# Kernel tuning notes

Measured on AMD Instinct MI355X. Metric: run time of the kernel, lower is better.

The kernel has to match this reference:

```python
import jax, jax.numpy as jnp
import numpy as np

B, N, D, S = 128, 1024, 512, 64
ITERS = 3
EPS = 1e-8


def setup_inputs() -> dict:
    key = jax.random.key(0)
    ks = jax.random.split(key, 10)
    inp = {
        "inputs_pe": jax.random.normal(ks[0], (B, N, D), dtype=jnp.float32),
        "inputs": jax.random.normal(ks[1], (B, N, D), dtype=jnp.float32),
        "slots": jax.random.normal(ks[2], (1, S, D), dtype=jnp.float32),
        "W1": jax.random.normal(ks[3], (D, D), dtype=jnp.float32) * 0.02,
        "b1": jnp.zeros((D,), dtype=jnp.float32),
        "W2": jax.random.normal(ks[4], (D, D), dtype=jnp.float32) * 0.02,
        "b2": jnp.zeros((D,), dtype=jnp.float32),
        "W3": jax.random.normal(ks[5], (D, D), dtype=jnp.float32) * 0.02,
        "b3": jnp.zeros((D,), dtype=jnp.float32),
    }
    return inp


def reference(inputs_pe, inputs, slots, W1, b1, W2, b2, W3, b3):
    b = inputs_pe.shape[0]
    scale = D ** (-0.5)
    # to_k: Linear -> ReLU -> Linear -> ReLU -> Linear (torch Linear: x @ W.T + b)
    h = jax.nn.relu(jnp.einsum('bnd,ed->bne', inputs_pe, W1) + b1)
    h = jax.nn.relu(jnp.einsum('bnd,ed->bne', h, W2) + b2)
    k = jnp.einsum('bnd,ed->bne', h, W3) + b3  # [b, n, d]

    q = jnp.broadcast_to(slots, (b, S, D))  # slots never updated in the loop
    for _ in range(ITERS):
        dots = jnp.einsum('bid,bjd->bij', q, k) * scale  # [b, S, n]
        s_j = dots.sum(axis=2, keepdims=True)            # sum over keys j -> [b, S, 1]
        s_all = dots.sum(axis=(1, 2), keepdims=True)     # total per batch -> [b, 1, 1]
        dots = dots / s_j * s_all
        attn = jax.nn.sigmoid(dots)
        attn2 = attn / (attn.sum(axis=-1, keepdims=True) + EPS)
        updates = jnp.einsum('bjd,bij->bid', inputs, attn2)  # [b, S, d]
    return updates, attn
```

## Files before the change

### kernel.cpp

```cpp
#include <hip/hip_runtime.h>
#include <stdint.h>

#define Bb 128
#define Nn 1024
#define Dd 512
#define Ss 64

constexpr float kScale = 0.044194173824159216f;
constexpr float kEps = 1e-8f;

typedef __bf16 bf16x8 __attribute__((ext_vector_type(8)));
typedef float f32x4 __attribute__((ext_vector_type(4)));
typedef float f32x16 __attribute__((ext_vector_type(16)));
typedef unsigned short ushort8 __attribute__((ext_vector_type(8)));

#define MFMA32 __builtin_amdgcn_mfma_f32_32x32x16_bf16

__device__ inline unsigned short f2bf_rne(float x) {
  unsigned u = __builtin_bit_cast(unsigned, x);
  u += 0x7FFFu + ((u >> 16) & 1u);
  return (unsigned short)(u >> 16);
}
__device__ inline float bf2f(unsigned short h) {
  unsigned u = ((unsigned)h) << 16;
  return __builtin_bit_cast(float, u);
}

__device__ inline void gl_lds16(const void* g, void* l) {
  typedef unsigned int u32;
  auto gp = (u32 __attribute__((address_space(1)))*)(unsigned long long)(uintptr_t)g;
  auto lp = (u32 __attribute__((address_space(3)))*)(unsigned int)(uintptr_t)l;
  __builtin_amdgcn_global_load_lds(gp, lp, 16, 0, 0);
}

__global__ void cast_split_i(const float* __restrict__ in,
                             unsigned short* __restrict__ out, int n8) {
  int i = blockIdx.x * blockDim.x + threadIdx.x;
  const int stride = gridDim.x * blockDim.x;
  for (; i < n8; i += stride) {
    const float4 v0 = ((const float4*)in)[i * 2];
    const float4 v1 = ((const float4*)in)[i * 2 + 1];
    float f[8] = {v0.x, v0.y, v0.z, v0.w, v1.x, v1.y, v1.z, v1.w};
    ushort8 h, lo;
#pragma unroll
    for (int j = 0; j < 8; j++) {
      h[j] = f2bf_rne(f[j]);
      lo[j] = f2bf_rne(f[j] - bf2f(h[j]));
    }
    ((ushort8*)out)[i * 2] = h;
    ((ushort8*)out)[i * 2 + 1] = lo;
  }
}

template <int ACT>
__global__ __launch_bounds__(512, 1) void gemm_hp(
    const unsigned short* __restrict__ A, const unsigned short* __restrict__ W,
    const float* __restrict__ bias, unsigned short* __restrict__ C) {
  constexpr int NH = 32;
  extern __shared__ unsigned short lds[];
  const int t = threadIdx.x, l = t & 63, w = t >> 6;
  const int wr = w >> 2, wc = w & 3;

  const int wg = ((blockIdx.x & 7) << 7) + (blockIdx.x >> 3);
  const long rowA0 = (long)(wg >> 1) * 256;
  const int colB0 = (wg & 1) * 256;

  const unsigned short* base8 = (w < 4) ? A + rowA0 * 1024 : W + (long)colB0 * 1024;
  const int p2s = ((l >> 1) ^ (l >> 4)) & 1;
  const unsigned short* srcp[4];
  int dstp[4];
#pragma unroll
  for (int j = 0; j < 4; j++) {
    const int cid = (w & 3) * 4 + j;
    srcp[j] = base8 + (long)(cid * 16 + (l >> 2)) * 1024 + p2s * 16 + (l & 1) * 8;
    dstp[j] = (w * 4 + j) * 512;
  }
#define STG(h)                                                            \
  {                                                                       \
    unsigned short* bq_ = lds + ((h) & 3) * 16384;                        \
    _Pragma("unroll") for (int j = 0; j < 4; j++)                         \
        gl_lds16(srcp[j] + (h) * 32, bq_ + dstp[j]);                      \
  }

  const int pp16 = (((l >> 5) ^ ((l >> 2) & 1))) * 16;
  const int abase0 = (wr * 128 + (l & 31)) * 32 + pp16;
  const int bbase0 = 8192 + (wc * 64 + (l & 31)) * 32 + pp16;

#define READF(h, S)                                                       \
  {                                                                       \
    const unsigned short* bq_ = lds + ((h) & 3) * 16384;                  \
    _Pragma("unroll") for (int m = 0; m < 4; m++) {                       \
      ah##S[m] = *(const bf16x8*)(bq_ + abase0 + m * 1024);               \
      al##S[m] = *(const bf16x8*)(bq_ + abase0 + m * 1024 + 8);           \
    }                                                                     \
    _Pragma("unroll") for (int n = 0; n < 2; n++) {                       \
      bh##S[n] = *(const bf16x8*)(bq_ + bbase0 + n * 1024);               \
      bl##S[n] = *(const bf16x8*)(bq_ + bbase0 + n * 1024 + 8);           \
    }                                                                     \
  }

#define MFMACL(S)                                                         \
  {                                                                       \
    _Pragma("unroll") for (int m = 0; m < 4; m++)                         \
        _Pragma("unroll") for (int n = 0; n < 2; n++) {                   \
      acc[m][n] = MFMA32(ah##S[m], bh##S[n], acc[m][n], 0, 0, 0);         \
      acc[m][n] = MFMA32(al##S[m], bh##S[n], acc[m][n], 0, 0, 0);         \
      acc[m][n] = MFMA32(ah##S[m], bl##S[n], acc[m][n], 0, 0, 0);         \
    }                                                                     \
  }

#define BODY(h, CUR, NXT)                                                 \
  {                                                                       \
    asm volatile("s_waitcnt lgkmcnt(0)" ::: "memory");                    \
    __builtin_amdgcn_sched_barrier(0);                                    \
    if ((h) < 29) {                                                       \
      asm volatile("s_waitcnt vmcnt(8)" ::: "memory");                    \
    } else if ((h) == 29) {                                               \
      asm volatile("s_waitcnt vmcnt(4)" ::: "memory");                    \
    } else if ((h) == 30) {                                               \
      asm volatile("s_waitcnt vmcnt(0)" ::: "memory");                    \
    }                                                                     \
    __builtin_amdgcn_s_barrier();                                         \
    if ((h) + 4 < NH) STG((h) + 4);                                       \
    if ((h) + 1 < NH) READF((h) + 1, NXT);                                \
    __builtin_amdgcn_sched_barrier(0);                                    \
    __builtin_amdgcn_s_setprio(1);                                        \
    MFMACL(CUR);                                                          \
    __builtin_amdgcn_s_setprio(0);                                        \
  }

  f32x16 acc[4][2] = {};
  bf16x8 ahA[4], alA[4], bhA[2], blA[2];
  bf16x8 ahB[4], alB[4], bhB[2], blB[2];

  STG(0); STG(1); STG(2); STG(3);
  asm volatile("s_waitcnt vmcnt(12)" ::: "memory");
  __builtin_amdgcn_s_barrier();
  READF(0, A);

  for (int hh = 0; hh < NH; hh += 2) {
    BODY(hh, A, B);
    BODY(hh + 1, B, A);
  }
#undef STG
#undef READF
#undef MFMACL
#undef BODY

#pragma unroll
  for (int m = 0; m < 4; m++)
#pragma unroll
    for (int n = 0; n < 2; n++) {
      const int col = colB0 + wc * 64 + n * 32 + (l & 31);
      const float bv = bias[col];
      const int cofs = (col >> 3) * 16 + (col & 7);
#pragma unroll
      for (int r = 0; r < 16; r++) {
        const long row = rowA0 + wr * 128 + m * 32 + (r & 3) + 8 * (r >> 2) + 4 * (l >> 5);
        float xv = acc[m][n][r] + bv;
        if (ACT) xv = fmaxf(xv, 0.0f);
        const unsigned short h = f2bf_rne(xv);
        unsigned short* cp = C + row * 1024 + cofs;
        cp[0] = h;
        cp[8] = f2bf_rne(xv - bf2f(h));
      }
    }
}

__global__ __launch_bounds__(256) void gemm_dots_split(
    const unsigned short* __restrict__ QI, const unsigned short* __restrict__ KI,
    float* __restrict__ dots) {
  constexpr int K = 512, BM = 64, BN = 128, BK = 32;
  __shared__ __align__(16) unsigned short lah[BM * BK];
  __shared__ __align__(16) unsigned short lal[BM * BK];
  __shared__ __align__(16) unsigned short lbh[BN * BK];
  __shared__ __align__(16) unsigned short lbl[BN * BK];
  const int t = threadIdx.x, l = t & 63, w = t >> 6;
  const int b = blockIdx.x >> 3, bc = blockIdx.x & 7;
  const unsigned short* kb = KI + (long)b * Nn * 1024;
  f32x4 acc[4][2] = {};

  const int qbase = (t >> 2) * 1024 + (t & 3) * 16;
  const long kbase0 = (long)(bc * BN + (t >> 2)) * 1024 + (t & 3) * 16;
  const long kbase1 = (long)(bc * BN + 64 + (t >> 2)) * 1024 + (t & 3) * 16;

  for (int k0 = 0; k0 < K; k0 += BK) {
    const int ko = k0 * 2;
    const int lo = w * 512;
    gl_lds16(QI + qbase + ko, lah + lo);
    gl_lds16(QI + qbase + ko + 8, lal + lo);
    gl_lds16(kb + kbase0 + ko, lbh + lo);
    gl_lds16(kb + kbase0 + ko + 8, lbl + lo);
    gl_lds16(kb + kbase1 + ko, lbh + 2048 + lo);
    gl_lds16(kb + kbase1 + ko + 8, lbl + 2048 + lo);
    __syncthreads();
    bf16x8 ah[4], al[4], bh[2], bl[2];
#pragma unroll
    for (int m = 0; m < 4; m++) {
      const int off = (m * 16 + (l & 15)) * BK + (l >> 4) * 8;
      ah[m] = *(const bf16x8*)(lah + off);
      al[m] = *(const bf16x8*)(lal + off);
    }
#pragma unroll
    for (int n = 0; n < 2; n++) {
      const int off = (w * 32 + n * 16 + (l & 15)) * BK + (l >> 4) * 8;
      bh[n] = *(const bf16x8*)(lbh + off);
      bl[n] = *(const bf16x8*)(lbl + off);
    }
#pragma unroll
    for (int m = 0; m < 4; m++)
#pragma unroll
      for (int n = 0; n < 2; n++) {
        acc[m][n] = __builtin_amdgcn_mfma_f32_16x16x32_bf16(ah[m], bh[n], acc[m][n], 0, 0, 0);
        acc[m][n] = __builtin_amdgcn_mfma_f32_16x16x32_bf16(al[m], bh[n], acc[m][n], 0, 0, 0);
        acc[m][n] = __builtin_amdgcn_mfma_f32_16x16x32_bf16(ah[m], bl[n], acc[m][n], 0, 0, 0);
      }
    __syncthreads();
  }
  float* dp = dots + (long)b * Ss * Nn;
#pragma unroll
  for (int m = 0; m < 4; m++) {
    const int row = m * 16 + (l >> 4) * 4;
#pragma unroll
    for (int n = 0; n < 2; n++) {
      const int col = bc * BN + w * 32 + n * 16 + (l & 15);
#pragma unroll
      for (int r = 0; r < 4; r++) dp[(long)(row + r) * Nn + col] = acc[m][n][r] * kScale;
    }
  }
}

__global__ __launch_bounds__(256) void reduce_k(
    const float* __restrict__ dots, float* __restrict__ s_j, float* __restrict__ s_all) {
  const int b = blockIdx.x;
  const int t = threadIdx.x;
  const float* dp = dots + (long)b * Ss * Nn;
  const int i = t >> 2, qq = t & 3;
  float s = 0.f;
  const float* rp = dp + i * Nn + qq * 256;
  for (int j = 0; j < 256; j++) s += rp[j];
  __shared__ float part[256];
  __shared__ float rowsum[64];
  part[t] = s;
  __syncthreads();
  if (t < 64) {
    const float v = part[t * 4] + part[t * 4 + 1] + part[t * 4 + 2] + part[t * 4 + 3];
    rowsum[t] = v;
    s_j[b * 64 + t] = v;
  }
  __syncthreads();
  if (t == 0) {
    float tot = 0.f;
    for (int k = 0; k < 64; k++) tot += rowsum[k];
    s_all[b] = tot;
  }
}

__global__ __launch_bounds__(256) void attn_k(
    const float* __restrict__ dots, const float* __restrict__ s_j,
    const float* __restrict__ s_all, float* __restrict__ attn_out,
    float* __restrict__ inv_r) {
  const int bi = blockIdx.x;
  const int b = bi >> 6;
  const int t = threadIdx.x;
  const float ratio = s_all[b] / s_j[bi];
  const float* dp = dots + (long)bi * Nn;
  float* ap = attn_out + (long)bi * Nn;
  float s = 0.f;
#pragma unroll
  for (int qq = 0; qq < 4; qq++) {
    const int j = qq * 256 + t;
    const float x = dp[j] * ratio;
    const float a = 1.f / (1.f + expf(-x));
    ap[j] = a;
    s += a;
  }
  __shared__ float red[256];
  red[t] = s;
  __syncthreads();
  for (int off = 128; off > 0; off >>= 1) {
    if (t < off) red[t] += red[t + off];
    __syncthreads();
  }
  if (t == 0) inv_r[bi] = 1.f / (red[0] + kEps);
}

__global__ __launch_bounds__(256, 1) void updates_k2(
    const float* __restrict__ attn, const float* __restrict__ inputs,
    const float* __restrict__ inv_r, float* __restrict__ out0) {
  constexpr int NT2 = 32;
  constexpr int BUF_F = 10240;
  extern __shared__ float ldsf[];
  const int t = threadIdx.x, lam = t & 63, w = t >> 6;
  const int b = blockIdx.x >> 1, dt = blockIdx.x & 1;
  const int ig = t >> 5, dg = t & 31;
  const float* inb = inputs + (size_t)b * (Nn * Dd) + dt * 256;
  const float* attsrc = attn + (size_t)b * (Ss * Nn) + (size_t)(t >> 2) * Nn + (t & 3) * 8;
  float acc[8][8] = {};
  float4 ga0, ga1, gb0, gb1;

#define UISSUE(bufi, tile, G0, G1)                                        \
  {                                                                       \
    const int j0_ = (tile)*32;                                            \
    G0 = *(const float4*)(attsrc + j0_);                                  \
    G1 = *(const float4*)(attsrc + j0_ + 4);                              \
    float* db_ = ldsf + (bufi)*BUF_F;                                     \
    _Pragma("unroll") for (int i_ = 0; i_ < 8; i_++) {                    \
      const int row_ = i_ * 4 + w;                                        \
      gl_lds16(inb + (size_t)(j0_ + row_) * Dd + lam * 4, db_ + row_ * 256); \
    }                                                                     \
  }

#define UWRITE(bufi, G0, G1)                                              \
  {                                                                       \
    float* ab_ = ldsf + (bufi)*BUF_F + 8192;                              \
    const int col_ = t >> 2;                                              \
    const int r0_ = (t & 3) * 8;                                          \
    ab_[(r0_ + 0) * 64 + col_] = G0.x;                                    \
    ab_[(r0_ + 1) * 64 + col_] = G0.y;                                    \
    ab_[(r0_ + 2) * 64 + col_] = G0.z;                                    \
    ab_[(r0_ + 3) * 64 + col_] = G0.w;                                    \
    ab_[(r0_ + 4) * 64 + col_] = G1.x;                                    \
    ab_[(r0_ + 5) * 64 + col_] = G1.y;                                    \
    ab_[(r0_ + 6) * 64 + col_] = G1.z;                                    \
    ab_[(r0_ + 7) * 64 + col_] = G1.w;                                    \
  }

#define UCOMP(bufi)                                                       \
  {                                                                       \
    const float* db_ = ldsf + (bufi)*BUF_F;                               \
    const float* ab_ = db_ + 8192;                                        \
    _Pragma("unroll 4") for (int jj = 0; jj < 32; jj++) {                 \
      float av[8], vv[8];                                                 \
      *(float4*)&av[0] = *(const float4*)(ab_ + jj * 64 + ig * 8);        \
      *(float4*)&av[4] = *(const float4*)(ab_ + jj * 64 + ig * 8 + 4);    \
      *(float4*)&vv[0] = *(const float4*)(db_ + jj * 256 + dg * 8);       \
      *(float4*)&vv[4] = *(const float4*)(db_ + jj * 256 + dg * 8 + 4);   \
      _Pragma("unroll") for (int m_ = 0; m_ < 8; m_++)                    \
          _Pragma("unroll") for (int n_ = 0; n_ < 8; n_++)                \
              acc[m_][n_] = __builtin_fmaf(av[m_], vv[n_], acc[m_][n_]);  \
    }                                                                     \
  }

  UISSUE(0, 0, ga0, ga1);
  UISSUE(1, 1, gb0, gb1);
  UWRITE(0, ga0, ga1);

  for (int tt = 0; tt < NT2; tt += 2) {
    asm volatile("s_waitcnt vmcnt(10)" ::: "memory");
    UWRITE((tt + 1) % 3, gb0, gb1);
    asm volatile("s_waitcnt lgkmcnt(0)" ::: "memory");
    __builtin_amdgcn_s_barrier();
    __builtin_amdgcn_sched_barrier(0);
    if (tt < NT2 - 2) UISSUE((tt + 2) % 3, tt + 2, ga0, ga1);
    UCOMP(tt % 3);
    if (tt + 1 < NT2 - 1) {
      asm volatile("s_waitcnt vmcnt(10)" ::: "memory");
    } else {
      asm volatile("s_waitcnt vmcnt(0)" ::: "memory");
    }
    if (tt + 1 < NT2 - 1) UWRITE((tt + 2) % 3, ga0, ga1);
    asm volatile("s_waitcnt lgkmcnt(0)" ::: "memory");
    __builtin_amdgcn_s_barrier();
    __builtin_amdgcn_sched_barrier(0);
    if (tt + 1 < NT2 - 2) UISSUE((tt + 3) % 3, tt + 3, gb0, gb1);
    UCOMP((tt + 1) % 3);
  }
#undef UISSUE
#undef UWRITE
#undef UCOMP

#pragma unroll
  for (int m = 0; m < 8; m++) {
    const int i = ig * 8 + m;
    const float ir = inv_r[b * 64 + i];
    float4 o0, o1;
    o0.x = acc[m][0] * ir; o0.y = acc[m][1] * ir; o0.z = acc[m][2] * ir; o0.w = acc[m][3] * ir;
    o1.x = acc[m][4] * ir; o1.y = acc[m][5] * ir; o1.z = acc[m][6] * ir; o1.w = acc[m][7] * ir;
    float* op = out0 + (size_t)(b * 64 + i) * Dd + dt * 256 + dg * 8;
    *(float4*)op = o0;
    *(float4*)(op + 4) = o1;
  }
}

extern "C" void kernel_launch(void* const* d_in, const int* in_sizes, int n_in,
                              void* d_out, int out_size, void* d_ws, size_t ws_size,
                              hipStream_t stream) {
  (void)in_sizes; (void)n_in; (void)out_size; (void)ws_size;
  const float* inputs_pe = (const float*)d_in[0];
  const float* inputs = (const float*)d_in[1];
  const float* slots = (const float*)d_in[2];
  const float* W1 = (const float*)d_in[3];
  const float* b1 = (const float*)d_in[4];
  const float* W2 = (const float*)d_in[5];
  const float* b2 = (const float*)d_in[6];
  const float* W3 = (const float*)d_in[7];
  const float* b3 = (const float*)d_in[8];

  char* ws = (char*)d_ws;
  size_t off = 0;
  auto alloc = [&](size_t bytes) -> void* {
    void* p = ws + off;
    off += (bytes + 255) & ~(size_t)255;
    return p;
  };
  const size_t actB = (size_t)Bb * Nn * 1024 * 2;
  unsigned short* AI = (unsigned short*)alloc(actB);
  unsigned short* BI = (unsigned short*)alloc(actB);
  unsigned short* w1i = (unsigned short*)alloc(Dd * 1024 * 2);
  unsigned short* w2i = (unsigned short*)alloc(Dd * 1024 * 2);
  unsigned short* w3i = (unsigned short*)alloc(Dd * 1024 * 2);
  unsigned short* qi = (unsigned short*)alloc(Ss * 1024 * 2);
  float* dotsb = (float*)alloc((size_t)Bb * Ss * Nn * 4);
  float* s_j = (float*)alloc(Bb * Ss * 4);
  float* s_all = (float*)alloc(Bb * 4);
  float* inv_r = (float*)alloc(Bb * Ss * 4);

  float* out_updates = (float*)d_out;
  float* out_attn = out_updates + (size_t)Bb * Ss * Dd;

  const int kLdsG = 4 * 32 * 1024;
  const int kLdsU = 3 * 40 * 1024;
  hipFuncSetAttribute(reinterpret_cast<const void*>(gemm_hp<1>),
                      hipFuncAttributeMaxDynamicSharedMemorySize, kLdsG);
  hipFuncSetAttribute(reinterpret_cast<const void*>(gemm_hp<0>),
                      hipFuncAttributeMaxDynamicSharedMemorySize, kLdsG);
  hipFuncSetAttribute(reinterpret_cast<const void*>(updates_k2),
                      hipFuncAttributeMaxDynamicSharedMemorySize, kLdsU);

  cast_split_i<<<4096, 256, 0, stream>>>(inputs_pe, AI, Bb * Nn * Dd / 8);
  cast_split_i<<<128, 256, 0, stream>>>(W1, w1i, Dd * Dd / 8);
  cast_split_i<<<128, 256, 0, stream>>>(W2, w2i, Dd * Dd / 8);
  cast_split_i<<<128, 256, 0, stream>>>(W3, w3i, Dd * Dd / 8);
  cast_split_i<<<16, 256, 0, stream>>>(slots, qi, Ss * Dd / 8);

  gemm_hp<1><<<1024, 512, kLdsG, stream>>>(AI, w1i, b1, BI);
  gemm_hp<1><<<1024, 512, kLdsG, stream>>>(BI, w2i, b2, AI);
  gemm_hp<0><<<1024, 512, kLdsG, stream>>>(AI, w3i, b3, BI);

  gemm_dots_split<<<Bb * 8, 256, 0, stream>>>(qi, BI, dotsb);
  reduce_k<<<Bb, 256, 0, stream>>>(dotsb, s_j, s_all);
  attn_k<<<Bb * Ss, 256, 0, stream>>>(dotsb, s_j, s_all, out_attn, inv_r);
  updates_k2<<<Bb * 2, 256, kLdsU, stream>>>(out_attn, inputs, inv_r, out_updates);
}
```

Baseline: 1.030 ms.

## Shrink GEMM and updates tiles, restructure reduce with wave shuffles

The three MLP GEMMs move from 256x256 tiles on 512-thread blocks to 128x128 tiles on 256-thread blocks with two blocks per CU, and the LDS swizzle is changed to match. The updates kernel now splits D into four 128-wide slices over 16-row tiles, so it launches more blocks with a smaller LDS footprint. The reduce kernel switches to coalesced float4 row reads with wavefront shuffle reductions. The aim is more parallelism and occupancy and less uncoalesced reading, at the cost of less data reuse per tile in the GEMMs and more redundant attention loads in the updates kernel.

```diff
diff --git a/kernel.cpp b/kernel.cpp
--- a/kernel.cpp
+++ b/kernel.cpp
@@ -53,55 +53,57 @@
 }
 
 template <int ACT>
-__global__ __launch_bounds__(512, 1) void gemm_hp(
+__global__ __launch_bounds__(256, 2) void gemm_tp(
     const unsigned short* __restrict__ A, const unsigned short* __restrict__ W,
     const float* __restrict__ bias, unsigned short* __restrict__ C) {
   constexpr int NH = 32;
   extern __shared__ unsigned short lds[];
   const int t = threadIdx.x, l = t & 63, w = t >> 6;
-  const int wr = w >> 2, wc = w & 3;
-
-  const int wg = ((blockIdx.x & 7) << 7) + (blockIdx.x >> 3);
-  const long rowA0 = (long)(wg >> 1) * 256;
-  const int colB0 = (wg & 1) * 256;
-
-  const unsigned short* base8 = (w < 4) ? A + rowA0 * 1024 : W + (long)colB0 * 1024;
-  const int p2s = ((l >> 1) ^ (l >> 4)) & 1;
+  const int wr = w >> 1, wc = w & 1;
+
+  const int wg = ((blockIdx.x & 7) << 9) + (blockIdx.x >> 3);
+  const long rowA0 = (long)(wg >> 2) * 128;
+  const int colB0 = (wg & 3) * 128;
+
+  const unsigned short* pbase =
+      (w < 2) ? A + rowA0 * 1024 : W + (long)colB0 * 1024;
+  const int qs = (l & 3) ^ ((l >> 3) & 3);
   const unsigned short* srcp[4];
   int dstp[4];
 #pragma unroll
   for (int j = 0; j < 4; j++) {
-    const int cid = (w & 3) * 4 + j;
-    srcp[j] = base8 + (long)(cid * 16 + (l >> 2)) * 1024 + p2s * 16 + (l & 1) * 8;
-    dstp[j] = (w * 4 + j) * 512;
+    const int cid = w * 4 + j;
+    const int rloc = (cid & 7) * 16 + (l >> 2);
+    srcp[j] = pbase + (long)rloc * 1024 + qs * 8;
+    dstp[j] = cid * 512;
   }
 #define STG(h)                                                            \
   {                                                                       \
-    unsigned short* bq_ = lds + ((h) & 3) * 16384;                        \
+    unsigned short* bq_ = lds + ((h) & 3) * 8192;                         \
     _Pragma("unroll") for (int j = 0; j < 4; j++)                         \
         gl_lds16(srcp[j] + (h) * 32, bq_ + dstp[j]);                      \
   }
 
-  const int pp16 = (((l >> 5) ^ ((l >> 2) & 1))) * 16;
-  const int abase0 = (wr * 128 + (l & 31)) * 32 + pp16;
-  const int bbase0 = 8192 + (wc * 64 + (l & 31)) * 32 + pp16;
+  const int ppA = ((2 * (l >> 5)) ^ ((l >> 1) & 3)) * 8;
+  const int ar = (wr * 64 + (l & 31)) * 32 + ppA;
+  const int br = 4096 + (wc * 64 + (l & 31)) * 32 + ppA;
 
 #define READF(h, S)                                                       \
   {                                                                       \
-    const unsigned short* bq_ = lds + ((h) & 3) * 16384;                  \
-    _Pragma("unroll") for (int m = 0; m < 4; m++) {                       \
-      ah##S[m] = *(const bf16x8*)(bq_ + abase0 + m * 1024);               \
-      al##S[m] = *(const bf16x8*)(bq_ + abase0 + m * 1024 + 8);           \
+    const unsigned short* bq_ = lds + ((h) & 3) * 8192;                   \
+    _Pragma("unroll") for (int m = 0; m < 2; m++) {                       \
+      ah##S[m] = *(const bf16x8*)(bq_ + (ar + m * 1024));                 \
+      al##S[m] = *(const bf16x8*)(bq_ + ((ar + m * 1024) ^ 8));           \
     }                                                                     \
     _Pragma("unroll") for (int n = 0; n < 2; n++) {                       \
-      bh##S[n] = *(const bf16x8*)(bq_ + bbase0 + n * 1024);               \
-      bl##S[n] = *(const bf16x8*)(bq_ + bbase0 + n * 1024 + 8);           \
+      bh##S[n] = *(const bf16x8*)(bq_ + (br + n * 1024));                 \
+      bl##S[n] = *(const bf16x8*)(bq_ + ((br + n * 1024) ^ 8));           \
     }                                                                     \
   }
 
 #define MFMACL(S)                                                         \
   {                                                                       \
-    _Pragma("unroll") for (int m = 0; m < 4; m++)                         \
+    _Pragma("unroll") for (int m = 0; m < 2; m++)                         \
         _Pragma("unroll") for (int n = 0; n < 2; n++) {                   \
       acc[m][n] = MFMA32(ah##S[m], bh##S[n], acc[m][n], 0, 0, 0);         \
       acc[m][n] = MFMA32(al##S[m], bh##S[n], acc[m][n], 0, 0, 0);         \
@@ -129,9 +131,9 @@
     __builtin_amdgcn_s_setprio(0);                                        \
   }
 
-  f32x16 acc[4][2] = {};
-  bf16x8 ahA[4], alA[4], bhA[2], blA[2];
-  bf16x8 ahB[4], alB[4], bhB[2], blB[2];
+  f32x16 acc[2][2] = {};
+  bf16x8 ahA[2], alA[2], bhA[2], blA[2];
+  bf16x8 ahB[2], alB[2], bhB[2], blB[2];
 
   STG(0); STG(1); STG(2); STG(3);
   asm volatile("s_waitcnt vmcnt(12)" ::: "memory");
@@ -148,7 +150,7 @@
 #undef BODY
 
 #pragma unroll
-  for (int m = 0; m < 4; m++)
+  for (int m = 0; m < 2; m++)
 #pragma unroll
     for (int n = 0; n < 2; n++) {
       const int col = colB0 + wc * 64 + n * 32 + (l & 31);
@@ -156,7 +158,7 @@
       const int cofs = (col >> 3) * 16 + (col & 7);
 #pragma unroll
       for (int r = 0; r < 16; r++) {
-        const long row = rowA0 + wr * 128 + m * 32 + (r & 3) + 8 * (r >> 2) + 4 * (l >> 5);
+        const long row = rowA0 + wr * 64 + m * 32 + (r & 3) + 8 * (r >> 2) + 4 * (l >> 5);
         float xv = acc[m][n][r] + bv;
         if (ACT) xv = fmaxf(xv, 0.0f);
         const unsigned short h = f2bf_rne(xv);
@@ -232,27 +234,29 @@
 
 __global__ __launch_bounds__(256) void reduce_k(
     const float* __restrict__ dots, float* __restrict__ s_j, float* __restrict__ s_all) {
-  const int b = blockIdx.x;
-  const int t = threadIdx.x;
-  const float* dp = dots + (long)b * Ss * Nn;
-  const int i = t >> 2, qq = t & 3;
-  float s = 0.f;
-  const float* rp = dp + i * Nn + qq * 256;
-  for (int j = 0; j < 256; j++) s += rp[j];
-  __shared__ float part[256];
+  const int b = blockIdx.x, t = threadIdx.x, l = t & 63, w = t >> 6;
+  const float4* dp = (const float4*)(dots + (long)b * Ss * Nn);
+  __shared__ float rowacc[64][4];
   __shared__ float rowsum[64];
-  part[t] = s;
+  for (int r = 0; r < 64; ++r) {
+    const float4 v = dp[r * 256 + t];
+    float s = v.x + v.y + v.z + v.w;
+#pragma unroll
+    for (int off = 32; off; off >>= 1) s += __shfl_down(s, off);
+    if (l == 0) rowacc[r][w] = s;
+  }
   __syncthreads();
   if (t < 64) {
-    const float v = part[t * 4] + part[t * 4 + 1] + part[t * 4 + 2] + part[t * 4 + 3];
+    const float v = rowacc[t][0] + rowacc[t][1] + rowacc[t][2] + rowacc[t][3];
     rowsum[t] = v;
     s_j[b * 64 + t] = v;
   }
   __syncthreads();
-  if (t == 0) {
-    float tot = 0.f;
-    for (int k = 0; k < 64; k++) tot += rowsum[k];
-    s_all[b] = tot;
+  if (t < 64) {
+    float v = rowsum[t];
+#pragma unroll
+    for (int off = 32; off; off >>= 1) v += __shfl_down(v, off);
+    if (t == 0) s_all[b] = v;
   }
 }
 
@@ -285,85 +289,80 @@
   if (t == 0) inv_r[bi] = 1.f / (red[0] + kEps);
 }
 
-__global__ __launch_bounds__(256, 1) void updates_k2(
+__global__ __launch_bounds__(256) void updates_k3(
     const float* __restrict__ attn, const float* __restrict__ inputs,
     const float* __restrict__ inv_r, float* __restrict__ out0) {
-  constexpr int NT2 = 32;
-  constexpr int BUF_F = 10240;
+  constexpr int NT2 = 64;
+  constexpr int BUF_F = 3072;
   extern __shared__ float ldsf[];
-  const int t = threadIdx.x, lam = t & 63, w = t >> 6;
-  const int b = blockIdx.x >> 1, dt = blockIdx.x & 1;
+  const int t = threadIdx.x, l = t & 63, w = t >> 6;
+  const int b = blockIdx.x >> 2, dt = blockIdx.x & 3;
   const int ig = t >> 5, dg = t & 31;
-  const float* inb = inputs + (size_t)b * (Nn * Dd) + dt * 256;
-  const float* attsrc = attn + (size_t)b * (Ss * Nn) + (size_t)(t >> 2) * Nn + (t & 3) * 8;
-  float acc[8][8] = {};
-  float4 ga0, ga1, gb0, gb1;
-
-#define UISSUE(bufi, tile, G0, G1)                                        \
-  {                                                                       \
-    const int j0_ = (tile)*32;                                            \
-    G0 = *(const float4*)(attsrc + j0_);                                  \
-    G1 = *(const float4*)(attsrc + j0_ + 4);                              \
+  const float* inb = inputs + (size_t)b * (Nn * Dd) + dt * 128;
+  const float* attsrc = attn + (size_t)b * (Ss * Nn) + (size_t)(t >> 2) * Nn + (t & 3) * 4;
+  float acc[8][4] = {};
+  float4 ga, gb;
+
+#define UISSUE(bufi, tile, G)                                             \
+  {                                                                       \
+    const int j0_ = (tile)*16;                                            \
+    G = *(const float4*)(attsrc + j0_);                                   \
     float* db_ = ldsf + (bufi)*BUF_F;                                     \
-    _Pragma("unroll") for (int i_ = 0; i_ < 8; i_++) {                    \
-      const int row_ = i_ * 4 + w;                                        \
-      gl_lds16(inb + (size_t)(j0_ + row_) * Dd + lam * 4, db_ + row_ * 256); \
-    }                                                                     \
-  }
-
-#define UWRITE(bufi, G0, G1)                                              \
-  {                                                                       \
-    float* ab_ = ldsf + (bufi)*BUF_F + 8192;                              \
+    _Pragma("unroll") for (int i_ = 0; i_ < 2; i_++) {                    \
+      const int rb_ = i_ * 8 + w * 2;                                     \
+      gl_lds16(inb + (size_t)(j0_ + rb_ + (l >> 5)) * Dd + (l & 31) * 4,  \
+               db_ + rb_ * 128);                                          \
+    }                                                                     \
+  }
+
+#define UWRITE(bufi, G)                                                   \
+  {                                                                       \
+    float* ab_ = ldsf + (bufi)*BUF_F + 2048;                              \
     const int col_ = t >> 2;                                              \
-    const int r0_ = (t & 3) * 8;                                          \
-    ab_[(r0_ + 0) * 64 + col_] = G0.x;                                    \
-    ab_[(r0_ + 1) * 64 + col_] = G0.y;                                    \
-    ab_[(r0_ + 2) * 64 + col_] = G0.z;                                    \
-    ab_[(r0_ + 3) * 64 + col_] = G0.w;                                    \
-    ab_[(r0_ + 4) * 64 + col_] = G1.x;                                    \
-    ab_[(r0_ + 5) * 64 + col_] = G1.y;                                    \
-    ab_[(r0_ + 6) * 64 + col_] = G1.z;                                    \
-    ab_[(r0_ + 7) * 64 + col_] = G1.w;                                    \
+    const int r0_ = (t & 3) * 4;                                          \
+    ab_[(r0_ + 0) * 64 + col_] = G.x;                                     \
+    ab_[(r0_ + 1) * 64 + col_] = G.y;                                     \
+    ab_[(r0_ + 2) * 64 + col_] = G.z;                                     \
+    ab_[(r0_ + 3) * 64 + col_] = G.w;                                     \
   }
 
 #define UCOMP(bufi)                                                       \
   {                                                                       \
     const float* db_ = ldsf + (bufi)*BUF_F;                               \
-    const float* ab_ = db_ + 8192;                                        \
-    _Pragma("unroll 4") for (int jj = 0; jj < 32; jj++) {                 \
-      float av[8], vv[8];                                                 \
+    const float* ab_ = db_ + 2048;                                        \
+    _Pragma("unroll 4") for (int jj = 0; jj < 16; jj++) {                 \
+      float av[8], vv[4];                                                 \
       *(float4*)&av[0] = *(const float4*)(ab_ + jj * 64 + ig * 8);        \
       *(float4*)&av[4] = *(const float4*)(ab_ + jj * 64 + ig * 8 + 4);    \
-      *(float4*)&vv[0] = *(const float4*)(db_ + jj * 256 + dg * 8);       \
-      *(float4*)&vv[4] = *(const float4*)(db_ + jj * 256 + dg * 8 + 4);   \
+      *(float4*)&vv[0] = *(const float4*)(db_ + jj * 128 + dg * 4);       \
       _Pragma("unroll") for (int m_ = 0; m_ < 8; m_++)                    \
-          _Pragma("unroll") for (int n_ = 0; n_ < 8; n_++)                \
+          _Pragma("unroll") for (int n_ = 0; n_ < 4; n_++)                \
               acc[m_][n_] = __builtin_fmaf(av[m_], vv[n_], acc[m_][n_]);  \
     }                                                                     \
   }
 
-  UISSUE(0, 0, ga0, ga1);
-  UISSUE(1, 1, gb0, gb1);
-  UWRITE(0, ga0, ga1);
+  UISSUE(0, 0, ga);
+  UISSUE(1, 1, gb);
+  UWRITE(0, ga);
 
   for (int tt = 0; tt < NT2; tt += 2) {
-    asm volatile("s_waitcnt vmcnt(10)" ::: "memory");
-    UWRITE((tt + 1) % 3, gb0, gb1);
+    asm volatile("s_waitcnt vmcnt(3)" ::: "memory");
+    UWRITE((tt + 1) % 3, gb);
     asm volatile("s_waitcnt lgkmcnt(0)" ::: "memory");
     __builtin_amdgcn_s_barrier();
     __builtin_amdgcn_sched_barrier(0);
-    if (tt < NT2 - 2) UISSUE((tt + 2) % 3, tt + 2, ga0, ga1);
+    if (tt < NT2 - 2) UISSUE((tt + 2) % 3, tt + 2, ga);
     UCOMP(tt % 3);
     if (tt + 1 < NT2 - 1) {
-      asm volatile("s_waitcnt vmcnt(10)" ::: "memory");
+      asm volatile("s_waitcnt vmcnt(3)" ::: "memory");
     } else {
       asm volatile("s_waitcnt vmcnt(0)" ::: "memory");
     }
-    if (tt + 1 < NT2 - 1) UWRITE((tt + 2) % 3, ga0, ga1);
+    if (tt + 1 < NT2 - 1) UWRITE((tt + 2) % 3, ga);
     asm volatile("s_waitcnt lgkmcnt(0)" ::: "memory");
     __builtin_amdgcn_s_barrier();
     __builtin_amdgcn_sched_barrier(0);
-    if (tt + 1 < NT2 - 2) UISSUE((tt + 3) % 3, tt + 3, gb0, gb1);
+    if (tt + 1 < NT2 - 2) UISSUE((tt + 3) % 3, tt + 3, gb);
     UCOMP((tt + 1) % 3);
   }
 #undef UISSUE
@@ -374,12 +373,10 @@
   for (int m = 0; m < 8; m++) {
     const int i = ig * 8 + m;
     const float ir = inv_r[b * 64 + i];
-    float4 o0, o1;
-    o0.x = acc[m][0] * ir; o0.y = acc[m][1] * ir; o0.z = acc[m][2] * ir; o0.w = acc[m][3] * ir;
-    o1.x = acc[m][4] * ir; o1.y = acc[m][5] * ir; o1.z = acc[m][6] * ir; o1.w = acc[m][7] * ir;
-    float* op = out0 + (size_t)(b * 64 + i) * Dd + dt * 256 + dg * 8;
-    *(float4*)op = o0;
-    *(float4*)(op + 4) = o1;
+    float4 o;
+    o.x = acc[m][0] * ir; o.y = acc[m][1] * ir; o.z = acc[m][2] * ir; o.w = acc[m][3] * ir;
+    float* op = out0 + (size_t)(b * 64 + i) * Dd + dt * 128 + dg * 4;
+    *(float4*)op = o;
   }
 }
 
@@ -419,13 +416,13 @@
   float* out_updates = (float*)d_out;
   float* out_attn = out_updates + (size_t)Bb * Ss * Dd;
 
-  const int kLdsG = 4 * 32 * 1024;
-  const int kLdsU = 3 * 40 * 1024;
-  hipFuncSetAttribute(reinterpret_cast<const void*>(gemm_hp<1>),
+  const int kLdsG = 4 * 16 * 1024;
+  const int kLdsU = 3 * 12 * 1024;
+  hipFuncSetAttribute(reinterpret_cast<const void*>(gemm_tp<1>),
                       hipFuncAttributeMaxDynamicSharedMemorySize, kLdsG);
-  hipFuncSetAttribute(reinterpret_cast<const void*>(gemm_hp<0>),
+  hipFuncSetAttribute(reinterpret_cast<const void*>(gemm_tp<0>),
                       hipFuncAttributeMaxDynamicSharedMemorySize, kLdsG);
-  hipFuncSetAttribute(reinterpret_cast<const void*>(updates_k2),
+  hipFuncSetAttribute(reinterpret_cast<const void*>(updates_k3),
                       hipFuncAttributeMaxDynamicSharedMemorySize, kLdsU);
 
   cast_split_i<<<4096, 256, 0, stream>>>(inputs_pe, AI, Bb * Nn * Dd / 8);
@@ -434,12 +431,12 @@
   cast_split_i<<<128, 256, 0, stream>>>(W3, w3i, Dd * Dd / 8);
   cast_split_i<<<16, 256, 0, stream>>>(slots, qi, Ss * Dd / 8);
 
-  gemm_hp<1><<<1024, 512, kLdsG, stream>>>(AI, w1i, b1, BI);
-  gemm_hp<1><<<1024, 512, kLdsG, stream>>>(BI, w2i, b2, AI);
-  gemm_hp<0><<<1024, 512, kLdsG, stream>>>(AI, w3i, b3, BI);
+  gemm_tp<1><<<4096, 256, kLdsG, stream>>>(AI, w1i, b1, BI);
+  gemm_tp<1><<<4096, 256, kLdsG, stream>>>(BI, w2i, b2, AI);
+  gemm_tp<0><<<4096, 256, kLdsG, stream>>>(AI, w3i, b3, BI);
 
   gemm_dots_split<<<Bb * 8, 256, 0, stream>>>(qi, BI, dotsb);
   reduce_k<<<Bb, 256, 0, stream>>>(dotsb, s_j, s_all);
   attn_k<<<Bb * Ss, 256, 0, stream>>>(dotsb, s_j, s_all, out_attn, inv_r);
-  updates_k2<<<Bb * 2, 256, kLdsU, stream>>>(out_attn, inputs, inv_r, out_updates);
-}
+  updates_k3<<<Bb * 4, 256, kLdsU, stream>>>(out_attn, inputs, inv_r, out_updates);
+}
```

After: 1.169 ms. +13.5%, slower.
